# Kernel optimization log

Hardware: AMD Instinct MI355X
Metric: run time of the kernel (lower is better)

Reference implementation:

```python
import jax, jax.numpy as jnp
import numpy as np

B, T, D, H, NH, E, K = 8, 1024, 512, 2048, 8, 8, 31
LN_EPS = 1e-12  # espnet LayerNorm default
BN_EPS = 1e-5


def setup_inputs() -> dict:
    key = jax.random.key(0)
    ks = iter(jax.random.split(key, 64))
    nrm = lambda shape, s=0.02: jax.random.normal(next(ks), shape, jnp.float32) * s
    return dict(
        x=jax.random.normal(next(ks), (B, T, D), jnp.float32),
        mask=jnp.ones((B, 1, T), bool),
        dialectid=jax.random.randint(next(ks), (B,), 1, E + 1),  # 1-based dialect ids
        ln_ffmac_g=jnp.ones((D,), jnp.float32), ln_ffmac_b=jnp.zeros((D,), jnp.float32),
        w1_mac=nrm((D, H)), b1_mac=jnp.zeros((H,), jnp.float32),
        w2_mac=nrm((H, D)), b2_mac=jnp.zeros((D,), jnp.float32),
        ln_mha_g=jnp.ones((D,), jnp.float32), ln_mha_b=jnp.zeros((D,), jnp.float32),
        wq=nrm((D, D)), bq=jnp.zeros((D,), jnp.float32),
        wk=nrm((D, D)), bk=jnp.zeros((D,), jnp.float32),
        wv=nrm((D, D)), bv=jnp.zeros((D,), jnp.float32),
        wo=nrm((D, D)), bo=jnp.zeros((D,), jnp.float32),
        ln_conv_g=jnp.ones((D,), jnp.float32), ln_conv_b=jnp.zeros((D,), jnp.float32),
        pw1_w=nrm((D, 2 * D)), pw1_b=jnp.zeros((2 * D,), jnp.float32),
        dw_w=nrm((D, 1, K)), dw_b=jnp.zeros((D,), jnp.float32),
        bn_g=jnp.ones((D,), jnp.float32), bn_b=jnp.zeros((D,), jnp.float32),
        bn_mean=jnp.zeros((D,), jnp.float32), bn_var=jnp.ones((D,), jnp.float32),
        pw2_w=nrm((D, D)), pw2_b=jnp.zeros((D,), jnp.float32),
        ln_ff_g=jnp.ones((D,), jnp.float32), ln_ff_b=jnp.zeros((D,), jnp.float32),
        gate_w=nrm((D, E)), gate_b=jnp.zeros((E,), jnp.float32),
        e_w1=nrm((E, D, H)), e_b1=jnp.zeros((E, H), jnp.float32),
        e_w2=nrm((E, H, D)), e_b2=jnp.zeros((E, D), jnp.float32),
        ln_final_g=jnp.ones((D,), jnp.float32), ln_final_b=jnp.zeros((D,), jnp.float32),
    )


def layer_norm(h, g, b):
    m = h.mean(-1, keepdims=True)
    v = ((h - m) ** 2).mean(-1, keepdims=True)
    return (h - m) * jax.lax.rsqrt(v + LN_EPS) * g + b


def mha(x, mask, wq, bq, wk, bk, wv, bv, wo, bo):
    dk = D // NH
    q = (x @ wq + bq).reshape(B, T, NH, dk)
    k = (x @ wk + bk).reshape(B, T, NH, dk)
    v = (x @ wv + bv).reshape(B, T, NH, dk)
    scores = jnp.einsum('bqhd,bkhd->bhqk', q, k) / jnp.sqrt(jnp.float32(dk))
    scores = jnp.where(mask[:, None, :, :], scores, jnp.float32(-1e9))  # [B,1,1,T] bcast
    attn = jax.nn.softmax(scores, axis=-1)
    o = jnp.einsum('bhqk,bkhd->bqhd', attn, v).reshape(B, T, D)
    return o @ wo + bo


def conv_module(x, pw1_w, pw1_b, dw_w, dw_b, bn_g, bn_b, bn_mean, bn_var, pw2_w, pw2_b):
    h = x @ pw1_w + pw1_b                                  # [B,T,2D]
    a, g = jnp.split(h, 2, axis=-1)
    h = a * jax.nn.sigmoid(g)                              # GLU -> [B,T,D]
    hc = jnp.transpose(h, (0, 2, 1))                       # [B,D,T]
    hc = jax.lax.conv_general_dilated(
        hc, dw_w, window_strides=(1,), padding=[(K // 2, K // 2)],
        dimension_numbers=('NCH', 'OIH', 'NCH'), feature_group_count=D)
    hc = hc + dw_b[None, :, None]
    h = jnp.transpose(hc, (0, 2, 1))                       # [B,T,D]
    h = (h - bn_mean) * jax.lax.rsqrt(bn_var + BN_EPS) * bn_g + bn_b  # BatchNorm (eval)
    h = h * jax.nn.sigmoid(h)                              # Swish
    return h @ pw2_w + pw2_b


def moe_ff(x, dialectid, gate_w, gate_b, e_w1, e_b1, e_w2, e_b2):
    probs = jax.nn.softmax(x.mean(1) @ gate_w + gate_b, axis=-1)   # [B,E]
    chosen = jnp.clip(dialectid - 1, 0, E - 1)                     # custom_expert_chosen
    w1 = e_w1[chosen]; b1 = e_b1[chosen]                           # gather [B,D,H]
    w2 = e_w2[chosen]; b2 = e_b2[chosen]
    h = jax.nn.relu(jnp.einsum('btd,bdh->bth', x, w1) + b1[:, None, :])
    y = jnp.einsum('bth,bhd->btd', h, w2) + b2[:, None, :]
    return y, probs, chosen


def reference(x, mask, dialectid,
              ln_ffmac_g, ln_ffmac_b, w1_mac, b1_mac, w2_mac, b2_mac,
              ln_mha_g, ln_mha_b, wq, bq, wk, bk, wv, bv, wo, bo,
              ln_conv_g, ln_conv_b, pw1_w, pw1_b, dw_w, dw_b,
              bn_g, bn_b, bn_mean, bn_var, pw2_w, pw2_b,
              ln_ff_g, ln_ff_b, gate_w, gate_b, e_w1, e_b1, e_w2, e_b2,
              ln_final_g, ln_final_b):
    ff_scale = 0.5  # macaron present
    # macaron feed-forward (pre-norm)
    residual = x
    h = layer_norm(x, ln_ffmac_g, ln_ffmac_b)
    h = jax.nn.relu(h @ w1_mac + b1_mac) @ w2_mac + b2_mac
    x = residual + ff_scale * h
    # self-attention
    residual = x
    h = layer_norm(x, ln_mha_g, ln_mha_b)
    x = residual + mha(h, mask, wq, bq, wk, bk, wv, bv, wo, bo)
    # convolution module
    residual = x
    h = layer_norm(x, ln_conv_g, ln_conv_b)
    x = residual + conv_module(h, pw1_w, pw1_b, dw_w, dw_b, bn_g, bn_b, bn_mean, bn_var, pw2_w, pw2_b)
    # MoE feed-forward
    residual = x
    h = layer_norm(x, ln_ff_g, ln_ff_b)
    h, expert_probs, expert_chosen = moe_ff(h, dialectid, gate_w, gate_b, e_w1, e_b1, e_w2, e_b2)
    x = residual + ff_scale * h
    # final norm (conv module present)
    x = layer_norm(x, ln_final_g, ln_final_b)
    return x
```

## Files before the change

kernel.cpp:

```cpp
#include <hip/hip_runtime.h>
#include <hip/hip_bf16.h>

constexpr int Bc = 8, Tc = 1024, Dc = 512, Hc = 2048, NHc = 8, DKc = 64, KC = 31;
constexpr long NTD = (long)Bc * Tc * Dc;

typedef short  bf16x8 __attribute__((ext_vector_type(8)));
typedef float  f32x4  __attribute__((ext_vector_type(4)));

__device__ __forceinline__ float bf2f(unsigned short u) {
  union { unsigned int i; float f; } c; c.i = ((unsigned int)u) << 16; return c.f;
}
__device__ __forceinline__ unsigned short f2bf(float f) {
  union { float f; unsigned int i; } c; c.f = f;
  unsigned int r = c.i + 0x7FFFu + ((c.i >> 16) & 1u);
  return (unsigned short)(r >> 16);
}
__device__ __forceinline__ float ldsc(const void* p, long i, int isbf) {
  return isbf ? bf2f(((const unsigned short*)p)[i]) : ((const float*)p)[i];
}
__device__ __forceinline__ void gl_lds16(const unsigned short* g, unsigned short* l) {
  __builtin_amdgcn_global_load_lds((const __attribute__((address_space(1))) void*)g,
                                   (__attribute__((address_space(3))) void*)l, 16, 0, 0);
}

__global__ void detect_k(const unsigned int* __restrict__ g, int* __restrict__ flag) {
  if (threadIdx.x == 0) flag[0] = (g[0] == 0x3F803F80u) ? 1 : 0;
}

__global__ __launch_bounds__(256) void cvt_k(const void* __restrict__ x,
                                             float* __restrict__ y, int n,
                                             const int* __restrict__ flag) {
  int isbf = flag[0];
  int i = blockIdx.x * 256 + threadIdx.x;
  if (i < n) y[i] = ldsc(x, i, isbf);
}

__global__ __launch_bounds__(256) void packb_k(const void* __restrict__ bq,
    const void* __restrict__ bk, const void* __restrict__ bv,
    float* __restrict__ o, const int* __restrict__ flag) {
  int isbf = flag[0];
  int i = blockIdx.x * 256 + threadIdx.x;
  const void* p = (i < 512) ? bq : ((i < 1024) ? bk : bv);
  o[i] = ldsc(p, i & 511, isbf);
}

__global__ __launch_bounds__(256) void transpose_k(const void* __restrict__ src_,
    unsigned short* __restrict__ dst, int K, int N,
    const int* __restrict__ dialectid, int batch0, const int* __restrict__ flag)
{
  int isbf = flag[0];
  long sofs = 0;
  if (dialectid) {
    int ex = dialectid[batch0 + blockIdx.z] - 1;
    ex = ex < 0 ? 0 : (ex > 7 ? 7 : ex);
    sofs = (long)ex * K * N;
    dst += (long)blockIdx.z * K * N;
  }
  __shared__ unsigned short t[32][36];
  int k0 = blockIdx.y * 32, n0 = blockIdx.x * 32;
  int r = threadIdx.x >> 3, c4 = (threadIdx.x & 7) * 4;
  long si = sofs + (long)(k0 + r) * N + n0 + c4;
  if (isbf) {
    ushort4 v = *reinterpret_cast<const ushort4*>((const unsigned short*)src_ + si);
    t[r][c4] = v.x; t[r][c4 + 1] = v.y; t[r][c4 + 2] = v.z; t[r][c4 + 3] = v.w;
  } else {
    float4 f = *reinterpret_cast<const float4*>((const float*)src_ + si);
    t[r][c4] = f2bf(f.x); t[r][c4 + 1] = f2bf(f.y);
    t[r][c4 + 2] = f2bf(f.z); t[r][c4 + 3] = f2bf(f.w);
  }
  __syncthreads();
  ushort4 o;
  o.x = t[c4 + 0][r]; o.y = t[c4 + 1][r]; o.z = t[c4 + 2][r]; o.w = t[c4 + 3][r];
  *reinterpret_cast<ushort4*>(dst + (long)(n0 + r) * K + k0 + c4) = o;
}

__global__ __launch_bounds__(256) void ln_k(const float* __restrict__ src,
    const void* __restrict__ g, const void* __restrict__ b,
    unsigned short* __restrict__ dst, const int* __restrict__ flag)
{
  int isbf = flag[0];
  int row = blockIdx.x;
  const float* p = src + (long)row * Dc;
  int tid = threadIdx.x;
  float x0 = p[tid], x1 = p[tid + 256];
  float s = x0 + x1, ss = x0 * x0 + x1 * x1;
#pragma unroll
  for (int off = 32; off; off >>= 1) { s += __shfl_xor(s, off); ss += __shfl_xor(ss, off); }
  __shared__ float rs[4], rss[4];
  int wave = tid >> 6, lane = tid & 63;
  if (lane == 0) { rs[wave] = s; rss[wave] = ss; }
  __syncthreads();
  s = rs[0] + rs[1] + rs[2] + rs[3];
  ss = rss[0] + rss[1] + rss[2] + rss[3];
  float mean = s * (1.0f / Dc);
  float var  = ss * (1.0f / Dc) - mean * mean;
  float inv  = rsqrtf(fmaxf(var, 0.0f) + 1e-12f);
  long base = (long)row * Dc;
  dst[base + tid]       = f2bf((x0 - mean) * inv * ldsc(g, tid, isbf)       + ldsc(b, tid, isbf));
  dst[base + tid + 256] = f2bf((x1 - mean) * inv * ldsc(g, tid + 256, isbf) + ldsc(b, tid + 256, isbf));
}

template<bool FINAL>
__global__ __launch_bounds__(256) void redln_k(float* x,
    const unsigned short* pb, long pplane, float scale,
    const void* __restrict__ g, const void* __restrict__ b,
    void* dst, const int* __restrict__ flag)
{
  int isbf = flag[0];
  int row = blockIdx.x;
  int tid = threadIdx.x;
  long base = (long)row * Dc;
  float x0 = x[base + tid]       + scale * (bf2f(pb[base + tid])       + bf2f(pb[pplane + base + tid]));
  float x1 = x[base + tid + 256] + scale * (bf2f(pb[base + tid + 256]) + bf2f(pb[pplane + base + tid + 256]));
  if (!FINAL) { x[base + tid] = x0; x[base + tid + 256] = x1; }
  float s = x0 + x1, ss = x0 * x0 + x1 * x1;
#pragma unroll
  for (int off = 32; off; off >>= 1) { s += __shfl_xor(s, off); ss += __shfl_xor(ss, off); }
  __shared__ float rs[4], rss[4];
  int wave = tid >> 6, lane = tid & 63;
  if (lane == 0) { rs[wave] = s; rss[wave] = ss; }
  __syncthreads();
  s = rs[0] + rs[1] + rs[2] + rs[3];
  ss = rss[0] + rss[1] + rss[2] + rss[3];
  float mean = s * (1.0f / Dc);
  float var  = ss * (1.0f / Dc) - mean * mean;
  float inv  = rsqrtf(fmaxf(var, 0.0f) + 1e-12f);
  float o0 = (x0 - mean) * inv * ldsc(g, tid, isbf)       + ldsc(b, tid, isbf);
  float o1 = (x1 - mean) * inv * ldsc(g, tid + 256, isbf) + ldsc(b, tid + 256, isbf);
  if (FINAL && !isbf) {
    ((float*)dst)[base + tid]       = o0;
    ((float*)dst)[base + tid + 256] = o1;
  } else {
    ((unsigned short*)dst)[base + tid]       = f2bf(o0);
    ((unsigned short*)dst)[base + tid + 256] = f2bf(o1);
  }
}

constexpr int EPI_STORE = 0, EPI_RELU = 1, EPI_ADD = 2, EPI_ADDHALF = 3,
              EPI_ROWDK = 4, EPI_DKROW = 5, EPI_ROWDK_Q = 6, EPI_QKV = 7,
              EPI_PART = 8;

template<int EPI, bool MOE, int SPLITK>
__global__ __launch_bounds__(256) void mgemm_k(
    const unsigned short* __restrict__ A,
    const unsigned short* __restrict__ BT,
    const void* __restrict__ bias,
    void* __restrict__ dst,
    int Kd, int N, const int* __restrict__ dialectid, int row_base,
    const int* __restrict__ flag, long pplane)
{
  int isbf = flag[0];
  __shared__ unsigned short As[3][128 * 32];
  __shared__ unsigned short Bs[3][128 * 32];
  int row0 = blockIdx.x * 128;
  int col0 = blockIdx.y * 128;
  const unsigned short* Bp = BT;
  long bofs = 0;
  if (MOE) {
    int bb = (row_base + row0) >> 10;
    int ex = dialectid[bb] - 1; ex = ex < 0 ? 0 : (ex > 7 ? 7 : ex);
    Bp += (long)(bb & 3) * (long)Kd * N;
    bofs = (long)ex * N;
  }
  int tid = threadIdx.x;
  int lane = tid & 63, wave = tid >> 6;
  int wm = (wave >> 1) * 64, wn = (wave & 1) * 64;
  int lm = lane & 15, quad = lane >> 4;
  int acol = ((lane & 3) ^ ((lane >> 3) & 3)) * 8;
  int rsl = (quad ^ ((lm >> 1) & 3)) * 8;

  f32x4 acc[4][4];
#pragma unroll
  for (int i = 0; i < 4; ++i)
#pragma unroll
    for (int j = 0; j < 4; ++j) acc[i][j] = (f32x4){0.f, 0.f, 0.f, 0.f};

  int kslice = Kd / SPLITK;
  int kbeg = (SPLITK > 1) ? (int)blockIdx.z * kslice : 0;
  int kend = kbeg + kslice;

  auto stage = [&](int buf, int k0) {
#pragma unroll
    for (int j = 0; j < 2; ++j) {
      int seg = wave * 2 + j;
      int r = seg * 16 + (lane >> 2);
      gl_lds16(A  + (long)(row0 + r) * Kd + k0 + acol, As[buf] + seg * 512);
      gl_lds16(Bp + (long)(col0 + r) * Kd + k0 + acol, Bs[buf] + seg * 512);
    }
  };

  stage(0, kbeg);
  if (kbeg + 32 < kend) {
    stage(1, kbeg + 32);
    asm volatile("s_waitcnt vmcnt(4)" ::: "memory");
  } else {
    asm volatile("s_waitcnt vmcnt(0)" ::: "memory");
  }
  __builtin_amdgcn_s_barrier();

  int cur = 0;
  for (int k0 = kbeg; k0 < kend; k0 += 32) {
    int pf = (k0 + 64 < kend);
    if (pf) {
      int nb = cur + 2; if (nb >= 3) nb -= 3;
      stage(nb, k0 + 64);
    }
    bf16x8 af[4], bfr[4];
#pragma unroll
    for (int t = 0; t < 4; ++t) {
      af[t]  = *reinterpret_cast<const bf16x8*>(As[cur] + (wm + t * 16 + lm) * 32 + rsl);
      bfr[t] = *reinterpret_cast<const bf16x8*>(Bs[cur] + (wn + t * 16 + lm) * 32 + rsl);
    }
    __builtin_amdgcn_s_setprio(1);
#pragma unroll
    for (int mt = 0; mt < 4; ++mt)
#pragma unroll
      for (int nt = 0; nt < 4; ++nt)
        acc[mt][nt] = __builtin_amdgcn_mfma_f32_16x16x32_bf16(af[mt], bfr[nt], acc[mt][nt], 0, 0, 0);
    __builtin_amdgcn_s_setprio(0);
    if (pf) asm volatile("s_waitcnt vmcnt(4)" ::: "memory");
    else    asm volatile("s_waitcnt vmcnt(0)" ::: "memory");
    __builtin_amdgcn_s_barrier();
    ++cur; if (cur >= 3) cur -= 3;
  }

  long zofs = (EPI == EPI_PART) ? (long)blockIdx.z * pplane : 0;
#pragma unroll
  for (int mt = 0; mt < 4; ++mt) {
#pragma unroll
    for (int nt = 0; nt < 4; ++nt) {
      int n = col0 + wn + nt * 16 + lm;
      float bv = (EPI == EPI_QKV) ? ((const float*)bias)[n]
                                  : ldsc(bias, bofs + n, isbf);
      if (SPLITK > 1 && blockIdx.z != 0) bv = 0.0f;
#pragma unroll
      for (int r = 0; r < 4; ++r) {
        int m = row0 + wm + mt * 16 + quad * 4 + r;
        float v = acc[mt][nt][r] + bv;
        if (EPI == EPI_STORE)
          ((unsigned short*)dst)[(long)m * N + n] = f2bf(v);
        else if (EPI == EPI_RELU)
          ((unsigned short*)dst)[(long)m * N + n] = f2bf(fmaxf(v, 0.0f));
        else if (EPI == EPI_PART)
          ((unsigned short*)dst)[zofs + (long)(row_base + m) * N + n] = f2bf(v);
        else if (EPI == EPI_ADD) {
          if (SPLITK == 1) ((float*)dst)[(long)m * N + n] += v;
          else             atomicAdd((float*)dst + ((long)m * N + n), v);
        } else if (EPI == EPI_ADDHALF) {
          if (SPLITK == 1) ((float*)dst)[(long)m * N + n] += 0.5f * v;
          else             atomicAdd((float*)dst + ((long)m * N + n), 0.5f * v);
        } else if (EPI == EPI_QKV) {
          int which = n >> 9, d = n & 511, hh = d >> 6, dd = d & 63;
          int bb = m >> 10, t = m & 1023;
          unsigned short* o = (unsigned short*)dst;
          if (which == 0)
            o[((long)(bb * NHc + hh) * Tc + t) * DKc + dd] = f2bf(v * 0.125f);
          else if (which == 1)
            o[4194304 + ((long)(bb * NHc + hh) * Tc + t) * DKc + dd] = f2bf(v);
          else
            o[8388608 + ((long)(bb * NHc + hh) * DKc + dd) * Tc + t] = f2bf(v);
        } else {
          int bb = m >> 10, t = m & 1023, hh = n >> 6, dd = n & 63;
          if (EPI == EPI_ROWDK)
            ((unsigned short*)dst)[((long)(bb * NHc + hh) * Tc + t) * DKc + dd] = f2bf(v);
          else if (EPI == EPI_ROWDK_Q)
            ((unsigned short*)dst)[((long)(bb * NHc + hh) * Tc + t) * DKc + dd] = f2bf(v * 0.125f);
          else
            ((unsigned short*)dst)[((long)(bb * NHc + hh) * DKc + dd) * Tc + t] = f2bf(v);
        }
      }
    }
  }
}

__global__ __launch_bounds__(256) void fattn_k(const unsigned short* __restrict__ q,
    const unsigned short* __restrict__ k, const unsigned short* __restrict__ vT,
    unsigned short* __restrict__ out)
{
  constexpr int PST = 72;
  __shared__ unsigned short ks[64 * PST];
  __shared__ unsigned short vs[64 * PST];
  __shared__ unsigned short plds[4][32][PST];
  int tid = threadIdx.x;
  int lane = tid & 63, wave = tid >> 6;
  int lm = lane & 15, quad = lane >> 4;
  int flat = blockIdx.x;
  int bh = ((flat >> 6) << 3) | (flat & 7);
  int qt = (flat >> 3) & 7;
  int trow0 = qt * 128 + wave * 32;
  long qbase = (long)bh * Tc * DKc;
  long vbase = (long)bh * DKc * Tc;

  int srow = tid >> 2, sseg = (tid & 3) * 16;

  bf16x8 aq[2][2];
#pragma unroll
  for (int mt = 0; mt < 2; ++mt)
#pragma unroll
    for (int s = 0; s < 2; ++s)
      aq[mt][s] = *reinterpret_cast<const bf16x8*>(
          q + qbase + (long)(trow0 + mt * 16 + lm) * DKc + s * 32 + quad * 8);

  f32x4 acc_o[2][4];
#pragma unroll
  for (int mt = 0; mt < 2; ++mt)
#pragma unroll
    for (int nt = 0; nt < 4; ++nt) acc_o[mt][nt] = (f32x4){0.f, 0.f, 0.f, 0.f};
  float lsum[2][4] = {{0.f, 0.f, 0.f, 0.f}, {0.f, 0.f, 0.f, 0.f}};

  float4 kr0 = *reinterpret_cast<const float4*>(k  + qbase + (long)srow * DKc + sseg);
  float4 kr1 = *reinterpret_cast<const float4*>(k  + qbase + (long)srow * DKc + sseg + 8);
  float4 vr0 = *reinterpret_cast<const float4*>(vT + vbase + (long)srow * Tc + sseg);
  float4 vr1 = *reinterpret_cast<const float4*>(vT + vbase + (long)srow * Tc + sseg + 8);

  for (int kt = 0; kt < Tc; kt += 64) {
    __syncthreads();
    *reinterpret_cast<float4*>(&ks[srow * PST + sseg])     = kr0;
    *reinterpret_cast<float4*>(&ks[srow * PST + sseg + 8]) = kr1;
    *reinterpret_cast<float4*>(&vs[srow * PST + sseg])     = vr0;
    *reinterpret_cast<float4*>(&vs[srow * PST + sseg + 8]) = vr1;
    __syncthreads();
    if (kt + 64 < Tc) {
      int kn = kt + 64;
      kr0 = *reinterpret_cast<const float4*>(k  + qbase + (long)(kn + srow) * DKc + sseg);
      kr1 = *reinterpret_cast<const float4*>(k  + qbase + (long)(kn + srow) * DKc + sseg + 8);
      vr0 = *reinterpret_cast<const float4*>(vT + vbase + (long)srow * Tc + kn + sseg);
      vr1 = *reinterpret_cast<const float4*>(vT + vbase + (long)srow * Tc + kn + sseg + 8);
    }
    f32x4 accs[2][4];
#pragma unroll
    for (int mt = 0; mt < 2; ++mt)
#pragma unroll
      for (int nt = 0; nt < 4; ++nt) accs[mt][nt] = (f32x4){0.f, 0.f, 0.f, 0.f};
#pragma unroll
    for (int s = 0; s < 2; ++s) {
#pragma unroll
      for (int nt = 0; nt < 4; ++nt) {
        bf16x8 bk = *reinterpret_cast<const bf16x8*>(&ks[(nt * 16 + lm) * PST + s * 32 + quad * 8]);
#pragma unroll
        for (int mt = 0; mt < 2; ++mt)
          accs[mt][nt] = __builtin_amdgcn_mfma_f32_16x16x32_bf16(aq[mt][s], bk, accs[mt][nt], 0, 0, 0);
      }
    }
#pragma unroll
    for (int mt = 0; mt < 2; ++mt)
#pragma unroll
      for (int nt = 0; nt < 4; ++nt) {
#pragma unroll
        for (int r = 0; r < 4; ++r) {
          float p = __expf(accs[mt][nt][r]);
          lsum[mt][r] += p;
          plds[wave][mt * 16 + quad * 4 + r][nt * 16 + lm] = f2bf(p);
        }
      }
#pragma unroll
    for (int s = 0; s < 2; ++s) {
      bf16x8 ap0 = *reinterpret_cast<const bf16x8*>(&plds[wave][lm][s * 32 + quad * 8]);
      bf16x8 ap1 = *reinterpret_cast<const bf16x8*>(&plds[wave][16 + lm][s * 32 + quad * 8]);
#pragma unroll
      for (int nt = 0; nt < 4; ++nt) {
        bf16x8 bv = *reinterpret_cast<const bf16x8*>(&vs[(nt * 16 + lm) * PST + s * 32 + quad * 8]);
        acc_o[0][nt] = __builtin_amdgcn_mfma_f32_16x16x32_bf16(ap0, bv, acc_o[0][nt], 0, 0, 0);
        acc_o[1][nt] = __builtin_amdgcn_mfma_f32_16x16x32_bf16(ap1, bv, acc_o[1][nt], 0, 0, 0);
      }
    }
  }
  int bb = bh >> 3, hh = bh & 7;
#pragma unroll
  for (int mt = 0; mt < 2; ++mt) {
#pragma unroll
    for (int r = 0; r < 4; ++r) {
      float l = lsum[mt][r];
      l += __shfl_xor(l, 1);
      l += __shfl_xor(l, 2);
      l += __shfl_xor(l, 4);
      l += __shfl_xor(l, 8);
      float inv = 1.0f / l;
      int t = trow0 + mt * 16 + quad * 4 + r;
#pragma unroll
      for (int nt = 0; nt < 4; ++nt)
        out[((long)(bb * Tc + t)) * Dc + hh * DKc + nt * 16 + lm] = f2bf(acc_o[mt][nt][r] * inv);
    }
  }
}

__global__ __launch_bounds__(256) void glu_k(const unsigned short* __restrict__ h,
                                             unsigned short* __restrict__ o) {
  int i = blockIdx.x * 256 + threadIdx.x;
  int m = i >> 9, d = i & 511;
  float a = bf2f(h[(long)m * 1024 + d]);
  float g = bf2f(h[(long)m * 1024 + 512 + d]);
  o[i] = f2bf(a * (1.0f / (1.0f + expf(-g))));
}

constexpr int TT = 16;
__global__ __launch_bounds__(256) void dwconv_k(const unsigned short* __restrict__ src,
    const void* __restrict__ w,  const void* __restrict__ wb,
    const void* __restrict__ bng, const void* __restrict__ bnb,
    const void* __restrict__ bnm, const void* __restrict__ bnv,
    unsigned short* __restrict__ dst, const int* __restrict__ flag)
{
  int isbf = flag[0];
  long i = (long)blockIdx.x * 256 + threadIdx.x;
  int d  = (int)(i & 511);
  int tc = (int)((i >> 9) & 63);
  int b  = (int)(i >> 15);
  int t0 = tc * TT;
  const unsigned short* s = src + (long)b * Tc * Dc + d;

  float win[TT + KC - 1];
#pragma unroll
  for (int j = 0; j < TT + KC - 1; ++j) {
    int tt = t0 + j - 15;
    win[j] = ((unsigned)tt < (unsigned)Tc) ? bf2f(s[(long)tt * Dc]) : 0.0f;
  }
  float wreg[KC];
#pragma unroll
  for (int kk = 0; kk < KC; ++kk) wreg[kk] = ldsc(w, d * KC + kk, isbf);

  float bias  = ldsc(wb, d, isbf);
  float scale = ldsc(bng, d, isbf) * rsqrtf(ldsc(bnv, d, isbf) + 1e-5f);
  float bnmv  = ldsc(bnm, d, isbf);
  float bnbv  = ldsc(bnb, d, isbf);
  unsigned short* o = dst + (long)b * Tc * Dc + (long)t0 * Dc + d;
#pragma unroll
  for (int r = 0; r < TT; ++r) {
    float acc = bias;
#pragma unroll
    for (int kk = 0; kk < KC; ++kk) acc += win[r + kk] * wreg[kk];
    float v = (acc - bnmv) * scale + bnbv;
    v = v * (1.0f / (1.0f + expf(-v)));
    o[(long)r * Dc] = f2bf(v);
  }
}

extern "C" void kernel_launch(void* const* d_in, const int* in_sizes, int n_in,
                              void* d_out, int out_size, void* d_ws, size_t ws_size,
                              hipStream_t stream) {
  const int* dialectid = (const int*)d_in[2];
  auto P = [&](int i) { return (const void*)d_in[i]; };

  char* base = (char*)d_ws;
  float*          x_cur = (float*)base;
  unsigned short* hn    = (unsigned short*)(base + (16L << 20));
  unsigned short* wt    = (unsigned short*)(base + (24L << 20));
  unsigned short* wtmoe = (unsigned short*)(base + (32L << 20));
  unsigned short* hidF  = (unsigned short*)(base + (32L << 20));
  unsigned short* dyn   = (unsigned short*)(base + (48L << 20));
  int*            flag  = (int*)(base + (72L << 20));
  unsigned short* w1T  = wt;
  unsigned short* w2T  = wt + 1048576;
  unsigned short* wqT  = wt + 2097152;
  unsigned short* wkT  = wt + 2359296;
  unsigned short* wvT  = wt + 2621440;
  unsigned short* woT  = wt + 2883584;
  unsigned short* pw1T = wt + 3145728;
  unsigned short* pw2T = wt + 3670016;
  float*          qkvb = (float*)(wt + 3932160);

  unsigned short* pbMac = hn;
  const long      ppMac = 25165824;
  unsigned short* pbDyn = dyn;
  const long      ppDyn = 4194304;
  unsigned short* pbMoE = wt;
  const long      ppMoE = 20971520;

  dim3 blk(256);
  const int nElem = (int)NTD;

  detect_k<<<1, 64, 0, stream>>>((const unsigned int*)d_in[3], flag);
  cvt_k<<<nElem / 256, blk, 0, stream>>>(P(0), x_cur, nElem, flag);

  transpose_k<<<dim3(64, 16), blk, 0, stream>>>(P(5),  w1T,  512, 2048, nullptr, 0, flag);
  transpose_k<<<dim3(16, 64), blk, 0, stream>>>(P(7),  w2T,  2048, 512, nullptr, 0, flag);
  transpose_k<<<dim3(16, 16), blk, 0, stream>>>(P(11), wqT,  512, 512,  nullptr, 0, flag);
  transpose_k<<<dim3(16, 16), blk, 0, stream>>>(P(13), wkT,  512, 512,  nullptr, 0, flag);
  transpose_k<<<dim3(16, 16), blk, 0, stream>>>(P(15), wvT,  512, 512,  nullptr, 0, flag);
  transpose_k<<<dim3(16, 16), blk, 0, stream>>>(P(17), woT,  512, 512,  nullptr, 0, flag);
  transpose_k<<<dim3(32, 16), blk, 0, stream>>>(P(21), pw1T, 512, 1024, nullptr, 0, flag);
  transpose_k<<<dim3(16, 16), blk, 0, stream>>>(P(29), pw2T, 512, 512,  nullptr, 0, flag);
  packb_k<<<6, blk, 0, stream>>>(P(12), P(14), P(16), qkvb, flag);

  unsigned short* hid = dyn;
  unsigned short* qb  = dyn;
  unsigned short* kb  = dyn + 4194304;
  unsigned short* vb  = dyn + 8388608;
  unsigned short* pw1o = dyn;
  unsigned short* gluo = dyn + 8388608;

  ln_k<<<Bc * Tc, blk, 0, stream>>>(x_cur, P(3), P(4), hn, flag);
  mgemm_k<EPI_RELU, false, 1><<<dim3(64, 16), blk, 0, stream>>>(
      hn, w1T, P(6), hidF, 512, 2048, nullptr, 0, flag, 0L);
  mgemm_k<EPI_PART, false, 2><<<dim3(64, 4, 2), blk, 0, stream>>>(
      hidF, w2T, P(8), pbMac, 2048, 512, nullptr, 0, flag, ppMac);
  redln_k<false><<<Bc * Tc, blk, 0, stream>>>(x_cur, pbMac, ppMac, 0.5f, P(9), P(10), hn, flag);

  mgemm_k<EPI_QKV, false, 1><<<dim3(64, 12), blk, 0, stream>>>(
      hn, wqT, qkvb, qb, 512, 1536, nullptr, 0, flag, 0L);
  fattn_k<<<dim3(512), blk, 0, stream>>>(qb, kb, vb, hn);
  mgemm_k<EPI_PART, false, 2><<<dim3(64, 4, 2), blk, 0, stream>>>(
      hn, woT, P(18), pbDyn, 512, 512, nullptr, 0, flag, ppDyn);
  redln_k<false><<<Bc * Tc, blk, 0, stream>>>(x_cur, pbDyn, ppDyn, 1.0f, P(19), P(20), hn, flag);

  mgemm_k<EPI_STORE, false, 1><<<dim3(64, 8), blk, 0, stream>>>(hn, pw1T, P(22), pw1o, 512, 1024, nullptr, 0, flag, 0L);
  glu_k<<<nElem / 256, blk, 0, stream>>>(pw1o, gluo);
  dwconv_k<<<(int)(NTD / TT / 256), blk, 0, stream>>>(gluo, P(23), P(24), P(25), P(26), P(27), P(28), hn, flag);
  mgemm_k<EPI_PART, false, 2><<<dim3(64, 4, 2), blk, 0, stream>>>(
      hn, pw2T, P(30), pbDyn, 512, 512, nullptr, 0, flag, ppDyn);
  redln_k<false><<<Bc * Tc, blk, 0, stream>>>(x_cur, pbDyn, ppDyn, 1.0f, P(31), P(32), hn, flag);

  for (int c = 0; c < 2; ++c) {
    unsigned short* w1m = wtmoe;
    unsigned short* w2m = wtmoe + 4 * 1048576;
    transpose_k<<<dim3(64, 16, 4), blk, 0, stream>>>(P(35), w1m, 512, 2048, dialectid, c * 4, flag);
    transpose_k<<<dim3(16, 64, 4), blk, 0, stream>>>(P(37), w2m, 2048, 512, dialectid, c * 4, flag);
    mgemm_k<EPI_RELU, true, 1><<<dim3(32, 16), blk, 0, stream>>>(
        hn + (long)c * 4096 * 512, w1m, P(36), hid, 512, 2048, dialectid, c * 4096, flag, 0L);
    mgemm_k<EPI_PART, true, 2><<<dim3(32, 4, 2), blk, 0, stream>>>(
        hid, w2m, P(38), pbMoE, 2048, 512, dialectid, c * 4096, flag, ppMoE);
  }

  redln_k<true><<<Bc * Tc, blk, 0, stream>>>(x_cur, pbMoE, ppMoE, 0.5f, P(39), P(40), d_out, flag);
}
```

Before: 600.9 us.

## Fuse cvt into LN, GLU into dwconv, batch transposes, single-pass MoE

```diff
diff --git a/kernel.cpp b/kernel.cpp
--- a/kernel.cpp
+++ b/kernel.cpp
@@ -25,14 +25,6 @@
 
 __global__ void detect_k(const unsigned int* __restrict__ g, int* __restrict__ flag) {
   if (threadIdx.x == 0) flag[0] = (g[0] == 0x3F803F80u) ? 1 : 0;
-}
-
-__global__ __launch_bounds__(256) void cvt_k(const void* __restrict__ x,
-                                             float* __restrict__ y, int n,
-                                             const int* __restrict__ flag) {
-  int isbf = flag[0];
-  int i = blockIdx.x * 256 + threadIdx.x;
-  if (i < n) y[i] = ldsc(x, i, isbf);
 }
 
 __global__ __launch_bounds__(256) void packb_k(const void* __restrict__ bq,
@@ -74,15 +66,41 @@
   *reinterpret_cast<ushort4*>(dst + (long)(n0 + r) * K + k0 + c4) = o;
 }
 
-__global__ __launch_bounds__(256) void ln_k(const float* __restrict__ src,
-    const void* __restrict__ g, const void* __restrict__ b,
+struct TP5 { const void* s[5]; unsigned short* d[5]; };
+__global__ __launch_bounds__(256) void transpose5_k(TP5 p, const int* __restrict__ flag)
+{
+  int isbf = flag[0];
+  const void* src_ = p.s[blockIdx.z];
+  unsigned short* dst = p.d[blockIdx.z];
+  __shared__ unsigned short t[32][36];
+  int k0 = blockIdx.y * 32, n0 = blockIdx.x * 32;
+  int r = threadIdx.x >> 3, c4 = (threadIdx.x & 7) * 4;
+  long si = (long)(k0 + r) * 512 + n0 + c4;
+  if (isbf) {
+    ushort4 v = *reinterpret_cast<const ushort4*>((const unsigned short*)src_ + si);
+    t[r][c4] = v.x; t[r][c4 + 1] = v.y; t[r][c4 + 2] = v.z; t[r][c4 + 3] = v.w;
+  } else {
+    float4 f = *reinterpret_cast<const float4*>((const float*)src_ + si);
+    t[r][c4] = f2bf(f.x); t[r][c4 + 1] = f2bf(f.y);
+    t[r][c4 + 2] = f2bf(f.z); t[r][c4 + 3] = f2bf(f.w);
+  }
+  __syncthreads();
+  ushort4 o;
+  o.x = t[c4 + 0][r]; o.y = t[c4 + 1][r]; o.z = t[c4 + 2][r]; o.w = t[c4 + 3][r];
+  *reinterpret_cast<ushort4*>(dst + (long)(n0 + r) * 512 + k0 + c4) = o;
+}
+
+__global__ __launch_bounds__(256) void cvtln_k(const void* __restrict__ xin,
+    float* __restrict__ x, const void* __restrict__ g, const void* __restrict__ b,
     unsigned short* __restrict__ dst, const int* __restrict__ flag)
 {
   int isbf = flag[0];
   int row = blockIdx.x;
-  const float* p = src + (long)row * Dc;
   int tid = threadIdx.x;
-  float x0 = p[tid], x1 = p[tid + 256];
+  long base = (long)row * Dc;
+  float x0 = ldsc(xin, base + tid, isbf);
+  float x1 = ldsc(xin, base + tid + 256, isbf);
+  x[base + tid] = x0; x[base + tid + 256] = x1;
   float s = x0 + x1, ss = x0 * x0 + x1 * x1;
 #pragma unroll
   for (int off = 32; off; off >>= 1) { s += __shfl_xor(s, off); ss += __shfl_xor(ss, off); }
@@ -95,7 +113,6 @@
   float mean = s * (1.0f / Dc);
   float var  = ss * (1.0f / Dc) - mean * mean;
   float inv  = rsqrtf(fmaxf(var, 0.0f) + 1e-12f);
-  long base = (long)row * Dc;
   dst[base + tid]       = f2bf((x0 - mean) * inv * ldsc(g, tid, isbf)       + ldsc(b, tid, isbf));
   dst[base + tid + 256] = f2bf((x1 - mean) * inv * ldsc(g, tid + 256, isbf) + ldsc(b, tid + 256, isbf));
 }
@@ -136,9 +153,8 @@
   }
 }
 
-constexpr int EPI_STORE = 0, EPI_RELU = 1, EPI_ADD = 2, EPI_ADDHALF = 3,
-              EPI_ROWDK = 4, EPI_DKROW = 5, EPI_ROWDK_Q = 6, EPI_QKV = 7,
-              EPI_PART = 8;
+constexpr int EPI_STORE = 0, EPI_RELU = 1,
+              EPI_QKV = 7, EPI_PART = 8;
 
 template<int EPI, bool MOE, int SPLITK>
 __global__ __launch_bounds__(256) void mgemm_k(
@@ -146,7 +162,7 @@
     const unsigned short* __restrict__ BT,
     const void* __restrict__ bias,
     void* __restrict__ dst,
-    int Kd, int N, const int* __restrict__ dialectid, int row_base,
+    int Kd, int N, const int* __restrict__ dialectid, int row_base, int bmask,
     const int* __restrict__ flag, long pplane)
 {
   int isbf = flag[0];
@@ -159,7 +175,7 @@
   if (MOE) {
     int bb = (row_base + row0) >> 10;
     int ex = dialectid[bb] - 1; ex = ex < 0 ? 0 : (ex > 7 ? 7 : ex);
-    Bp += (long)(bb & 3) * (long)Kd * N;
+    Bp += (long)(bb & bmask) * (long)Kd * N;
     bofs = (long)ex * N;
   }
   int tid = threadIdx.x;
@@ -243,13 +259,7 @@
           ((unsigned short*)dst)[(long)m * N + n] = f2bf(fmaxf(v, 0.0f));
         else if (EPI == EPI_PART)
           ((unsigned short*)dst)[zofs + (long)(row_base + m) * N + n] = f2bf(v);
-        else if (EPI == EPI_ADD) {
-          if (SPLITK == 1) ((float*)dst)[(long)m * N + n] += v;
-          else             atomicAdd((float*)dst + ((long)m * N + n), v);
-        } else if (EPI == EPI_ADDHALF) {
-          if (SPLITK == 1) ((float*)dst)[(long)m * N + n] += 0.5f * v;
-          else             atomicAdd((float*)dst + ((long)m * N + n), 0.5f * v);
-        } else if (EPI == EPI_QKV) {
+        else if (EPI == EPI_QKV) {
           int which = n >> 9, d = n & 511, hh = d >> 6, dd = d & 63;
           int bb = m >> 10, t = m & 1023;
           unsigned short* o = (unsigned short*)dst;
@@ -259,14 +269,6 @@
             o[4194304 + ((long)(bb * NHc + hh) * Tc + t) * DKc + dd] = f2bf(v);
           else
             o[8388608 + ((long)(bb * NHc + hh) * DKc + dd) * Tc + t] = f2bf(v);
-        } else {
-          int bb = m >> 10, t = m & 1023, hh = n >> 6, dd = n & 63;
-          if (EPI == EPI_ROWDK)
-            ((unsigned short*)dst)[((long)(bb * NHc + hh) * Tc + t) * DKc + dd] = f2bf(v);
-          else if (EPI == EPI_ROWDK_Q)
-            ((unsigned short*)dst)[((long)(bb * NHc + hh) * Tc + t) * DKc + dd] = f2bf(v * 0.125f);
-          else
-            ((unsigned short*)dst)[((long)(bb * NHc + hh) * DKc + dd) * Tc + t] = f2bf(v);
         }
       }
     }
@@ -384,17 +386,8 @@
   }
 }
 
-__global__ __launch_bounds__(256) void glu_k(const unsigned short* __restrict__ h,
-                                             unsigned short* __restrict__ o) {
-  int i = blockIdx.x * 256 + threadIdx.x;
-  int m = i >> 9, d = i & 511;
-  float a = bf2f(h[(long)m * 1024 + d]);
-  float g = bf2f(h[(long)m * 1024 + 512 + d]);
-  o[i] = f2bf(a * (1.0f / (1.0f + expf(-g))));
-}
-
 constexpr int TT = 16;
-__global__ __launch_bounds__(256) void dwconv_k(const unsigned short* __restrict__ src,
+__global__ __launch_bounds__(256) void dwconv_k(const unsigned short* __restrict__ pw1,
     const void* __restrict__ w,  const void* __restrict__ wb,
     const void* __restrict__ bng, const void* __restrict__ bnb,
     const void* __restrict__ bnm, const void* __restrict__ bnv,
@@ -406,13 +399,17 @@
   int tc = (int)((i >> 9) & 63);
   int b  = (int)(i >> 15);
   int t0 = tc * TT;
-  const unsigned short* s = src + (long)b * Tc * Dc + d;
+  const unsigned short* s = pw1 + (long)b * Tc * 1024 + d;
 
   float win[TT + KC - 1];
 #pragma unroll
   for (int j = 0; j < TT + KC - 1; ++j) {
     int tt = t0 + j - 15;
-    win[j] = ((unsigned)tt < (unsigned)Tc) ? bf2f(s[(long)tt * Dc]) : 0.0f;
+    if ((unsigned)tt < (unsigned)Tc) {
+      float a = bf2f(s[(long)tt * 1024]);
+      float g = bf2f(s[(long)tt * 1024 + 512]);
+      win[j] = a * (1.0f / (1.0f + expf(-g)));
+    } else win[j] = 0.0f;
   }
   float wreg[KC];
 #pragma unroll
@@ -440,14 +437,12 @@
   const int* dialectid = (const int*)d_in[2];
   auto P = [&](int i) { return (const void*)d_in[i]; };
 
+  bool sp = ws_size >= ((161L << 20) + 64);
+
   char* base = (char*)d_ws;
   float*          x_cur = (float*)base;
   unsigned short* hn    = (unsigned short*)(base + (16L << 20));
   unsigned short* wt    = (unsigned short*)(base + (24L << 20));
-  unsigned short* wtmoe = (unsigned short*)(base + (32L << 20));
-  unsigned short* hidF  = (unsigned short*)(base + (32L << 20));
-  unsigned short* dyn   = (unsigned short*)(base + (48L << 20));
-  int*            flag  = (int*)(base + (72L << 20));
   unsigned short* w1T  = wt;
   unsigned short* w2T  = wt + 1048576;
   unsigned short* wqT  = wt + 2097152;
@@ -458,66 +453,99 @@
   unsigned short* pw2T = wt + 3670016;
   float*          qkvb = (float*)(wt + 3932160);
 
-  unsigned short* pbMac = hn;
-  const long      ppMac = 25165824;
-  unsigned short* pbDyn = dyn;
-  const long      ppDyn = 4194304;
-  unsigned short* pbMoE = wt;
-  const long      ppMoE = 20971520;
+  unsigned short *hidF, *qb, *kb, *vb, *pw1o, *hid, *w1m, *w2m;
+  unsigned short *pbMac, *pbDyn, *pbMoE;
+  long ppMac, ppDyn, ppMoE;
+  int* flag;
+
+  if (sp) {
+    hidF = (unsigned short*)(base + (32L << 20));
+    hid  = hidF;
+    qb   = (unsigned short*)(base + (64L << 20));
+    kb   = qb + 4194304;
+    vb   = qb + 8388608;
+    pw1o = (unsigned short*)(base + (64L << 20));
+    pbMac = pbDyn = pbMoE = (unsigned short*)(base + (112L << 20));
+    ppMac = ppDyn = ppMoE = 4194304;
+    w1m  = (unsigned short*)(base + (128L << 20));
+    w2m  = (unsigned short*)(base + (144L << 20));
+    flag = (int*)(base + (160L << 20));
+  } else {
+    unsigned short* wtmoe = (unsigned short*)(base + (32L << 20));
+    hidF = (unsigned short*)(base + (32L << 20));
+    unsigned short* dyn = (unsigned short*)(base + (48L << 20));
+    hid  = dyn;
+    qb   = dyn;
+    kb   = dyn + 4194304;
+    vb   = dyn + 8388608;
+    pw1o = dyn;
+    w1m  = wtmoe;
+    w2m  = wtmoe + 4 * 1048576;
+    pbMac = hn;  ppMac = 25165824;
+    pbDyn = dyn; ppDyn = 4194304;
+    pbMoE = wt;  ppMoE = 20971520;
+    flag = (int*)(base + (72L << 20));
+  }
 
   dim3 blk(256);
   const int nElem = (int)NTD;
 
   detect_k<<<1, 64, 0, stream>>>((const unsigned int*)d_in[3], flag);
-  cvt_k<<<nElem / 256, blk, 0, stream>>>(P(0), x_cur, nElem, flag);
 
   transpose_k<<<dim3(64, 16), blk, 0, stream>>>(P(5),  w1T,  512, 2048, nullptr, 0, flag);
   transpose_k<<<dim3(16, 64), blk, 0, stream>>>(P(7),  w2T,  2048, 512, nullptr, 0, flag);
-  transpose_k<<<dim3(16, 16), blk, 0, stream>>>(P(11), wqT,  512, 512,  nullptr, 0, flag);
-  transpose_k<<<dim3(16, 16), blk, 0, stream>>>(P(13), wkT,  512, 512,  nullptr, 0, flag);
-  transpose_k<<<dim3(16, 16), blk, 0, stream>>>(P(15), wvT,  512, 512,  nullptr, 0, flag);
-  transpose_k<<<dim3(16, 16), blk, 0, stream>>>(P(17), woT,  512, 512,  nullptr, 0, flag);
   transpose_k<<<dim3(32, 16), blk, 0, stream>>>(P(21), pw1T, 512, 1024, nullptr, 0, flag);
-  transpose_k<<<dim3(16, 16), blk, 0, stream>>>(P(29), pw2T, 512, 512,  nullptr, 0, flag);
+  {
+    TP5 tp;
+    tp.s[0] = P(11); tp.d[0] = wqT;
+    tp.s[1] = P(13); tp.d[1] = wkT;
+    tp.s[2] = P(15); tp.d[2] = wvT;
+    tp.s[3] = P(17); tp.d[3] = woT;
+    tp.s[4] = P(29); tp.d[4] = pw2T;
+    transpose5_k<<<dim3(16, 16, 5), blk, 0, stream>>>(tp, flag);
+  }
   packb_k<<<6, blk, 0, stream>>>(P(12), P(14), P(16), qkvb, flag);
-
-  unsigned short* hid = dyn;
-  unsigned short* qb  = dyn;
-  unsigned short* kb  = dyn + 4194304;
-  unsigned short* vb  = dyn + 8388608;
-  unsigned short* pw1o = dyn;
-  unsigned short* gluo = dyn + 8388608;
-
-  ln_k<<<Bc * Tc, blk, 0, stream>>>(x_cur, P(3), P(4), hn, flag);
+  if (sp) {
+    transpose_k<<<dim3(64, 16, 8), blk, 0, stream>>>(P(35), w1m, 512, 2048, dialectid, 0, flag);
+    transpose_k<<<dim3(16, 64, 8), blk, 0, stream>>>(P(37), w2m, 2048, 512, dialectid, 0, flag);
+  }
+
+  cvtln_k<<<Bc * Tc, blk, 0, stream>>>(P(0), x_cur, P(3), P(4), hn, flag);
   mgemm_k<EPI_RELU, false, 1><<<dim3(64, 16), blk, 0, stream>>>(
-      hn, w1T, P(6), hidF, 512, 2048, nullptr, 0, flag, 0L);
+      hn, w1T, P(6), hidF, 512, 2048, nullptr, 0, 0, flag, 0L);
   mgemm_k<EPI_PART, false, 2><<<dim3(64, 4, 2), blk, 0, stream>>>(
-      hidF, w2T, P(8), pbMac, 2048, 512, nullptr, 0, flag, ppMac);
+      hidF, w2T, P(8), pbMac, 2048, 512, nullptr, 0, 0, flag, ppMac);
   redln_k<false><<<Bc * Tc, blk, 0, stream>>>(x_cur, pbMac, ppMac, 0.5f, P(9), P(10), hn, flag);
 
   mgemm_k<EPI_QKV, false, 1><<<dim3(64, 12), blk, 0, stream>>>(
-      hn, wqT, qkvb, qb, 512, 1536, nullptr, 0, flag, 0L);
+      hn, wqT, qkvb, qb, 512, 1536, nullptr, 0, 0, flag, 0L);
   fattn_k<<<dim3(512), blk, 0, stream>>>(qb, kb, vb, hn);
   mgemm_k<EPI_PART, false, 2><<<dim3(64, 4, 2), blk, 0, stream>>>(
-      hn, woT, P(18), pbDyn, 512, 512, nullptr, 0, flag, ppDyn);
+      hn, woT, P(18), pbDyn, 512, 512, nullptr, 0, 0, flag, ppDyn);
   redln_k<false><<<Bc * Tc, blk, 0, stream>>>(x_cur, pbDyn, ppDyn, 1.0f, P(19), P(20), hn, flag);
 
-  mgemm_k<EPI_STORE, false, 1><<<dim3(64, 8), blk, 0, stream>>>(hn, pw1T, P(22), pw1o, 512, 1024, nullptr, 0, flag, 0L);
-  glu_k<<<nElem / 256, blk, 0, stream>>>(pw1o, gluo);
-  dwconv_k<<<(int)(NTD / TT / 256), blk, 0, stream>>>(gluo, P(23), P(24), P(25), P(26), P(27), P(28), hn, flag);
+  mgemm_k<EPI_STORE, false, 1><<<dim3(64, 8), blk, 0, stream>>>(
+      hn, pw1T, P(22), pw1o, 512, 1024, nullptr, 0, 0, flag, 0L);
+  dwconv_k<<<(int)(NTD / TT / 256), blk, 0, stream>>>(
+      pw1o, P(23), P(24), P(25), P(26), P(27), P(28), hn, flag);
   mgemm_k<EPI_PART, false, 2><<<dim3(64, 4, 2), blk, 0, stream>>>(
-      hn, pw2T, P(30), pbDyn, 512, 512, nullptr, 0, flag, ppDyn);
+      hn, pw2T, P(30), pbDyn, 512, 512, nullptr, 0, 0, flag, ppDyn);
   redln_k<false><<<Bc * Tc, blk, 0, stream>>>(x_cur, pbDyn, ppDyn, 1.0f, P(31), P(32), hn, flag);
 
-  for (int c = 0; c < 2; ++c) {
-    unsigned short* w1m = wtmoe;
-    unsigned short* w2m = wtmoe + 4 * 1048576;
-    transpose_k<<<dim3(64, 16, 4), blk, 0, stream>>>(P(35), w1m, 512, 2048, dialectid, c * 4, flag);
-    transpose_k<<<dim3(16, 64, 4), blk, 0, stream>>>(P(37), w2m, 2048, 512, dialectid, c * 4, flag);
-    mgemm_k<EPI_RELU, true, 1><<<dim3(32, 16), blk, 0, stream>>>(
-        hn + (long)c * 4096 * 512, w1m, P(36), hid, 512, 2048, dialectid, c * 4096, flag, 0L);
-    mgemm_k<EPI_PART, true, 2><<<dim3(32, 4, 2), blk, 0, stream>>>(
-        hid, w2m, P(38), pbMoE, 2048, 512, dialectid, c * 4096, flag, ppMoE);
+  if (sp) {
+    mgemm_k<EPI_RELU, true, 1><<<dim3(64, 16), blk, 0, stream>>>(
+        hn, w1m, P(36), hid, 512, 2048, dialectid, 0, 7, flag, 0L);
+    mgemm_k<EPI_PART, true, 2><<<dim3(64, 4, 2), blk, 0, stream>>>(
+        hid, w2m, P(38), pbMoE, 2048, 512, dialectid, 0, 7, flag, ppMoE);
+  } else {
+    for (int c = 0; c < 2; ++c) {
+      transpose_k<<<dim3(64, 16, 4), blk, 0, stream>>>(P(35), w1m, 512, 2048, dialectid, c * 4, flag);
+      transpose_k<<<dim3(16, 64, 4), blk, 0, stream>>>(P(37), w2m, 2048, 512, dialectid, c * 4, flag);
+      mgemm_k<EPI_RELU, true, 1><<<dim3(32, 16), blk, 0, stream>>>(
+          hn + (long)c * 4096 * 512, w1m, P(36), hid, 512, 2048, dialectid, c * 4096, 3, flag, 0L);
+      mgemm_k<EPI_PART, true, 2><<<dim3(32, 4, 2), blk, 0, stream>>>(
+          hid, w2m, P(38), pbMoE, 2048, 512, dialectid, c * 4096, 3, flag, ppMoE);
+    }
   }
 
   redln_k<true><<<Bc * Tc, blk, 0, stream>>>(x_cur, pbMoE, ppMoE, 0.5f, P(39), P(40), d_out, flag);
```

New measurement: 541.6 us. 1.11x faster.
